# Performance work log

Hardware: AMD Instinct MI355X
Metric: run time of the kernel (lower is better)

## Reference

```python
import jax, jax.numpy as jnp
import numpy as np

N = 4096
HID = 512
NUM_HEADS = 8
HEAD_DIM = HID // NUM_HEADS
SCALING = HID ** (-0.5)


def setup_inputs() -> dict:
    key = jax.random.key(0)
    k0, k1, k2, k3, k4, k5 = jax.random.split(key, 6)
    h = jax.random.normal(k0, (N, HID), dtype=jnp.float32)
    A = (jax.random.uniform(k1, (N, N), dtype=jnp.float32) < 0.01).astype(jnp.float32)
    scale = 0.02
    Wq = jax.random.normal(k2, (HID, HID), dtype=jnp.float32) * scale
    Wk = jax.random.normal(k3, (HID, HID), dtype=jnp.float32) * scale
    Wv = jax.random.normal(k4, (HID, HID), dtype=jnp.float32) * scale
    Wo = jax.random.normal(k5, (HID, HID), dtype=jnp.float32) * scale
    return {"A": A, "h": h, "Wq": Wq, "Wk": Wk, "Wv": Wv, "Wo": Wo}


def reference(A, h, Wq, Wk, Wv, Wo):
    n = h.shape[0]
    # nn.Linear: y = x @ W.T ; reshape(N, head_dim, num_heads) puts heads LAST
    q = (h @ Wq.T).reshape(n, HEAD_DIM, NUM_HEADS) * SCALING  # [N, D, H]
    k = (h @ Wk.T).reshape(n, HEAD_DIM, NUM_HEADS)            # [N, D, H]
    v = (h @ Wv.T).reshape(n, HEAD_DIM, NUM_HEADS)            # [N, D, H]
    # scores = bmm(q^T[H,N,D], k^T[H,D,N]) -> [H, N, N]
    scores = jnp.einsum('ndh,mdh->hnm', q, k)
    # mask by dense multiply (zeros still contribute exp(0) to softmax, as in source)
    attn = jax.nn.softmax(A[None, :, :] * scores, axis=-1)    # [H, N, N]
    # out = bmm(attn, v^T[H,N,D]) -> [H, N, D] -> transpose to [N, D, H]
    out = jnp.einsum('hnm,mdh->ndh', attn, v)                 # [N, D, H]
    out = out.reshape(n, HEAD_DIM * NUM_HEADS) @ Wo.T         # [N, HID]
    return out
```

## Files before the change

### kernel.cpp

```cpp
#include <hip/hip_runtime.h>
#include <hip/hip_bf16.h>


#define N_TOK 4096
#define HID   512
#define NHEAD 8
#define HDIM  64
#define SCALING_F 0.044194173824159216f

#define QH_OFF    0u
#define KVB_OFF   2097152u
#define VSP_OFF   3145728u
#define VSUM_OFF  3162112u
#define CNT_OFF   3162624u
#define LIST_OFF  3166720u
#define HB_OFF    3691008u
#define WQKV_OFF  4739584u
#define WO_OFF    5132800u

typedef __attribute__((ext_vector_type(8))) short bf16x8;
typedef __attribute__((ext_vector_type(4))) float f32x4;
typedef __attribute__((ext_vector_type(2))) float f32x2;

__device__ __forceinline__ ushort f2bf(float f) {
    union { float f; unsigned u; } x; x.f = f;
    const unsigned r = x.u + 0x7fffu + ((x.u >> 16) & 1u);
    return (ushort)(r >> 16);
}

#define GLOAD_LDS16(g, l) \
    __builtin_amdgcn_global_load_lds((const __attribute__((address_space(1))) void*)(g), \
                                     (__attribute__((address_space(3))) void*)(l), 16, 0, 0)

__global__ __launch_bounds__(256) void prep(const float* __restrict__ A,
                                            const float* __restrict__ h,
                                            const float* __restrict__ wq,
                                            const float* __restrict__ wk,
                                            const float* __restrict__ wv,
                                            const float* __restrict__ wo,
                                            float* __restrict__ ws)
{
    const int bx = blockIdx.x;
    if (bx < 1024) {
        int* cnts  = (int*)(ws + CNT_OFF);
        int* lists = (int*)(ws + LIST_OFF);
        const int row  = bx * 4 + (threadIdx.x >> 6);
        const int lane = threadIdx.x & 63;
        const float4* Arow = (const float4*)(A + (size_t)row * N_TOK);
        int* out = lists + (size_t)row * 128;
        int cnt = 0;
#pragma unroll 4
        for (int it = 0; it < 16; ++it) {
            const float4 v = Arow[it * 64 + lane];
            const float vals[4] = {v.x, v.y, v.z, v.w};
#pragma unroll
            for (int j = 0; j < 4; ++j) {
                const bool nz = (vals[j] != 0.0f);
                const unsigned long long mask = __ballot(nz);
                if (nz) {
                    const int pos = cnt + __popcll(mask & ((1ull << lane) - 1ull));
                    if (pos < 128) out[pos] = it * 256 + lane * 4 + j;
                }
                cnt += __popcll(mask);
            }
        }
        if (lane == 0) cnts[row] = (cnt < 128) ? cnt : 128;
        return;
    }

    const int cb    = bx - 1024;
    const int chunk = cb >> 8;
    const int inner = (cb & 255) * 1024 + threadIdx.x * 4;
    ushort* hb    = (ushort*)(ws + HB_OFF);
    ushort* wqkvb = (ushort*)(ws + WQKV_OFF);
    ushort* wob   = (ushort*)(ws + WO_OFF);

    if (chunk < 11) {
        const float* src;
        ushort* dst;
        if (chunk < 8)       { src = h + (size_t)chunk * 262144; dst = hb + (size_t)chunk * 262144; }
        else if (chunk == 8) { src = wq; dst = wqkvb; }
        else if (chunk == 9) { src = wk; dst = wqkvb + 262144; }
        else                 { src = wv; dst = wqkvb + 524288; }
        const float4 v = *(const float4*)&src[inner];
        ushort4 o;
        o.x = f2bf(v.x); o.y = f2bf(v.y); o.z = f2bf(v.z); o.w = f2bf(v.w);
        *(ushort4*)&dst[inner] = o;
    } else {
        const float4 v = *(const float4*)&wo[inner];
        const int o = inner >> 9;
        const int j0 = inner & 511;
        const float vals[4] = {v.x, v.y, v.z, v.w};
#pragma unroll
        for (int jj = 0; jj < 4; ++jj) {
            const int j = j0 + jj;
            wob[o * 512 + (j & 7) * 64 + (j >> 3)] = f2bf(vals[jj]);
        }
    }
}

__global__ __launch_bounds__(256) void qkv_gemm_mfma(const float* __restrict__ ws_ro,
                                                     float* __restrict__ ws)
{
    const ushort* Xb = (const ushort*)(ws_ro + HB_OFF);
    const int z = blockIdx.z;
    const int hh = blockIdx.x;
    const ushort* W = (const ushort*)(ws_ro + WQKV_OFF) + (size_t)z * 262144;

    const int mb = blockIdx.y * 128;

    __shared__ ushort SM[12288];

    const int t    = threadIdx.x;
    const int w    = t >> 6;
    const int lane = t & 63;
    const int wr   = w >> 1, wc = w & 1;
    const int fr   = lane & 15;
    const int fq   = lane >> 4;
    const int fk   = fq * 8;

    const int srow = w * 16 + (lane >> 2);
    const int scol = (lane & 3) * 8;
    const ushort* gA = Xb + (size_t)(mb + srow) * HID + scol;
    const ushort* gB = W + (size_t)(hh + srow * 8) * HID + scol;

#define QKV_STAGE(p, kb) do { \
        ushort* base_ = &SM[(p) * 6144]; \
        GLOAD_LDS16(gA + (kb),            base_ + w * 512); \
        GLOAD_LDS16(gA + (kb) + 64 * HID, base_ + 2048 + w * 512); \
        GLOAD_LDS16(gB + (kb),            base_ + 4096 + w * 512); \
    } while (0)

    f32x4 acc[4][2] = {};

    QKV_STAGE(0, 0);
    __syncthreads();
    for (int ts = 0; ts < 16; ++ts) {
        const int p = ts & 1;
        if (ts < 15) QKV_STAGE(p ^ 1, (ts + 1) * 32);
        const ushort* base = &SM[p * 6144];
        bf16x8 a[4], b[2];
#pragma unroll
        for (int mi = 0; mi < 4; ++mi)
            a[mi] = *(const bf16x8*)&base[(wr * 64 + mi * 16 + fr) * 32 + fk];
#pragma unroll
        for (int ni = 0; ni < 2; ++ni)
            b[ni] = *(const bf16x8*)&base[4096 + (wc * 32 + ni * 16 + fr) * 32 + fk];
#pragma unroll
        for (int mi = 0; mi < 4; ++mi)
#pragma unroll
            for (int ni = 0; ni < 2; ++ni)
                acc[mi][ni] = __builtin_amdgcn_mfma_f32_16x16x32_bf16(a[mi], b[ni], acc[mi][ni], 0, 0, 0);
        __syncthreads();
    }
#undef QKV_STAGE

    if (z == 0) {
        float* Yh = ws + QH_OFF + (size_t)hh * (N_TOK * HDIM);
#pragma unroll
        for (int ni = 0; ni < 2; ++ni) {
            const int d = wc * 32 + ni * 16 + fr;
#pragma unroll
            for (int mi = 0; mi < 4; ++mi) {
                const int r0 = mb + wr * 64 + mi * 16 + fq * 4;
#pragma unroll
                for (int j = 0; j < 4; ++j)
                    Yh[(size_t)(r0 + j) * HDIM + d] = acc[mi][ni][j] * SCALING_F;
            }
        }
    } else {
        unsigned char* KVh = (unsigned char*)(ws + KVB_OFF)
                           + (size_t)hh * (N_TOK * 128) + ((z == 1) ? 0 : 8);
#pragma unroll
        for (int ni = 0; ni < 2; ++ni) {
            const int d = wc * 32 + ni * 16 + fr;
            const int doff = (d >> 3) * 16 + (d & 7);
#pragma unroll
            for (int mi = 0; mi < 4; ++mi) {
                const int r0 = mb + wr * 64 + mi * 16 + fq * 4;
#pragma unroll
                for (int j = 0; j < 4; ++j) {
                    const float v = acc[mi][ni][j];
                    const int p = __builtin_amdgcn_cvt_pk_fp8_f32(v, v, 0, false);
                    KVh[(size_t)(r0 + j) * 128 + doff] = (unsigned char)(p & 0xff);
                }
            }
        }
        if (z == 2) {
            float* red = (float*)SM;
#pragma unroll
            for (int ni = 0; ni < 2; ++ni) {
                float ps = 0.f;
#pragma unroll
                for (int mi = 0; mi < 4; ++mi)
#pragma unroll
                    for (int j = 0; j < 4; ++j) ps += acc[mi][ni][j];
                red[(wr * 4 + fq) * 64 + wc * 32 + ni * 16 + fr] = ps;
            }
            __syncthreads();
            if (t < 64) {
                float s = 0.f;
#pragma unroll
                for (int r = 0; r < 8; ++r) s += red[r * 64 + t];
                ws[VSP_OFF + blockIdx.y * 512 + hh * 64 + t] = s;
            }
        }
    }
}

__global__ __launch_bounds__(64) void vsum_collapse(float* __restrict__ ws)
{
    const float* VSP = ws + VSP_OFF;
    const int hh = blockIdx.x, d = threadIdx.x;
    float s = 0.f;
#pragma unroll
    for (int mb = 0; mb < 32; ++mb) s += VSP[mb * 512 + hh * 64 + d];
    ws[VSUM_OFF + hh * 64 + d] = s;
}

__global__ __launch_bounds__(256) void attn_sparse(float* __restrict__ ws)
{
    const int b    = blockIdx.x;
    const int n    = (b >> 3) * 4 + (b & 3);
    const int hg   = (b >> 2) & 1;
    const int t    = threadIdx.x;
    const int w    = t >> 6;
    const int lane = t & 63;
    const int g    = lane >> 3;
    const int dg   = lane & 7;
    const int h    = hg * 4 + w;

    const int* cnts  = (const int*)(ws + CNT_OFF);
    const int* lists = (const int*)(ws + LIST_OFF);

    __shared__ int s_idx[128];
    const int cnt = cnts[n];
    if (t < 128) s_idx[t] = (t < cnt) ? lists[(size_t)n * 128 + t] : 0;
    __syncthreads();

    const float* Qh = ws + QH_OFF;
    const unsigned char* kvh = (const unsigned char*)(ws + KVB_OFF)
                             + (size_t)h * (N_TOK * 128) + dg * 16;
    ushort* opb = (ushort*)(ws + HB_OFF);

    const float* qrow = Qh + ((size_t)h * N_TOK + n) * HDIM + dg * 8;
    const float4 qa = *(const float4*)qrow;
    const float4 qb = *(const float4*)(qrow + 4);

    float acc[8] = {0.f, 0.f, 0.f, 0.f, 0.f, 0.f, 0.f, 0.f};
    float den = 0.f;

    const int iters = (cnt + 7) >> 3;

#define ATTN_DOT(kw0, kw1, sval) do { \
        const f32x2 k0_ = __builtin_amdgcn_cvt_pk_f32_fp8((kw0), false); \
        const f32x2 k1_ = __builtin_amdgcn_cvt_pk_f32_fp8((kw0), true);  \
        const f32x2 k2_ = __builtin_amdgcn_cvt_pk_f32_fp8((kw1), false); \
        const f32x2 k3_ = __builtin_amdgcn_cvt_pk_f32_fp8((kw1), true);  \
        sval = qa.x * k0_[0] + qa.y * k0_[1] + qa.z * k1_[0] + qa.w * k1_[1] \
             + qb.x * k2_[0] + qb.y * k2_[1] + qb.z * k3_[0] + qb.w * k3_[1]; \
        sval += __shfl_xor(sval, 1); \
        sval += __shfl_xor(sval, 2); \
        sval += __shfl_xor(sval, 4); \
    } while (0)

#define ATTN_ACC(vw0, vw1, wgt) do { \
        const f32x2 v0_ = __builtin_amdgcn_cvt_pk_f32_fp8((vw0), false); \
        const f32x2 v1_ = __builtin_amdgcn_cvt_pk_f32_fp8((vw0), true);  \
        const f32x2 v2_ = __builtin_amdgcn_cvt_pk_f32_fp8((vw1), false); \
        const f32x2 v3_ = __builtin_amdgcn_cvt_pk_f32_fp8((vw1), true);  \
        acc[0] += (wgt) * v0_[0]; acc[1] += (wgt) * v0_[1]; \
        acc[2] += (wgt) * v1_[0]; acc[3] += (wgt) * v1_[1]; \
        acc[4] += (wgt) * v2_[0]; acc[5] += (wgt) * v2_[1]; \
        acc[6] += (wgt) * v3_[0]; acc[7] += (wgt) * v3_[1]; \
    } while (0)

    int i = 0;
    for (; i + 2 <= iters; i += 2) {
        const int j0 = i * 8 + g;
        const int j1 = j0 + 8;
        const int m0 = s_idx[j0];
        const int m1 = s_idx[j1];
        const uint4 kv0 = *(const uint4*)(kvh + (size_t)m0 * 128);
        const uint4 kv1 = *(const uint4*)(kvh + (size_t)m1 * 128);
        float s0, s1;
        ATTN_DOT(kv0.x, kv0.y, s0);
        ATTN_DOT(kv1.x, kv1.y, s1);
        const float w0 = (j0 < cnt) ? __expf(s0) - 1.0f : 0.0f;
        const float w1 = (j1 < cnt) ? __expf(s1) - 1.0f : 0.0f;
        ATTN_ACC(kv0.z, kv0.w, w0);
        ATTN_ACC(kv1.z, kv1.w, w1);
        den += w0;
        den += w1;
    }
    if (i < iters) {
        const int j0 = i * 8 + g;
        const int m0 = s_idx[j0 & 127];
        const uint4 kv0 = *(const uint4*)(kvh + (size_t)m0 * 128);
        float s0;
        ATTN_DOT(kv0.x, kv0.y, s0);
        const float w0 = (j0 < cnt) ? __expf(s0) - 1.0f : 0.0f;
        ATTN_ACC(kv0.z, kv0.w, w0);
        den += w0;
    }
#undef ATTN_DOT
#undef ATTN_ACC

#pragma unroll
    for (int off = 8; off <= 32; off <<= 1) {
#pragma unroll
        for (int e = 0; e < 8; ++e) acc[e] += __shfl_xor(acc[e], off);
        den += __shfl_xor(den, off);
    }

    if (g == 0) {
        const float* vsp = ws + VSUM_OFF + h * 64 + dg * 8;
        const float4 va = *(const float4*)vsp;
        const float4 vb = *(const float4*)(vsp + 4);
        const float vs[8] = {va.x, va.y, va.z, va.w, vb.x, vb.y, vb.z, vb.w};
        const float r = 1.0f / (4096.0f + den);
        bf16x8 o;
#pragma unroll
        for (int e = 0; e < 8; ++e) o[e] = (short)f2bf((vs[e] + acc[e]) * r);
        *(bf16x8*)(opb + (size_t)n * HID + h * 64 + dg * 8) = o;
    }
}

__global__ __launch_bounds__(256) void out_gemm_mfma(const float* __restrict__ ws_ro,
                                                     float* __restrict__ out)
{
    const ushort* Xb = (const ushort*)(ws_ro + HB_OFF);
    const ushort* W  = (const ushort*)(ws_ro + WO_OFF);

    const int nb = blockIdx.x * 64;
    const int mb = blockIdx.y * 128;

    __shared__ ushort SM[12288];

    const int t    = threadIdx.x;
    const int w    = t >> 6;
    const int lane = t & 63;
    const int wr   = w >> 1, wc = w & 1;
    const int fr   = lane & 15;
    const int fq   = lane >> 4;
    const int fk   = fq * 8;

    const int srow = w * 16 + (lane >> 2);
    const int scol = (lane & 3) * 8;
    const ushort* gA = Xb + (size_t)(mb + srow) * HID + scol;
    const ushort* gB = W  + (size_t)(nb + srow) * HID + scol;

#define OUT_STAGE(p, kb) do { \
        ushort* base_ = &SM[(p) * 6144]; \
        GLOAD_LDS16(gA + (kb),            base_ + w * 512); \
        GLOAD_LDS16(gA + (kb) + 64 * HID, base_ + 2048 + w * 512); \
        GLOAD_LDS16(gB + (kb),            base_ + 4096 + w * 512); \
    } while (0)

    f32x4 acc[4][2] = {};

    OUT_STAGE(0, 0);
    __syncthreads();
    for (int ts = 0; ts < 16; ++ts) {
        const int p = ts & 1;
        if (ts < 15) OUT_STAGE(p ^ 1, (ts + 1) * 32);
        const ushort* base = &SM[p * 6144];
        bf16x8 a[4], b[2];
#pragma unroll
        for (int mi = 0; mi < 4; ++mi)
            a[mi] = *(const bf16x8*)&base[(wr * 64 + mi * 16 + fr) * 32 + fk];
#pragma unroll
        for (int ni = 0; ni < 2; ++ni)
            b[ni] = *(const bf16x8*)&base[4096 + (wc * 32 + ni * 16 + fr) * 32 + fk];
#pragma unroll
        for (int mi = 0; mi < 4; ++mi)
#pragma unroll
            for (int ni = 0; ni < 2; ++ni)
                acc[mi][ni] = __builtin_amdgcn_mfma_f32_16x16x32_bf16(a[mi], b[ni], acc[mi][ni], 0, 0, 0);
        __syncthreads();
    }
#undef OUT_STAGE

#pragma unroll
    for (int ni = 0; ni < 2; ++ni) {
        const int col = nb + wc * 32 + ni * 16 + fr;
#pragma unroll
        for (int mi = 0; mi < 4; ++mi) {
            const int r0 = mb + wr * 64 + mi * 16 + fq * 4;
#pragma unroll
            for (int j = 0; j < 4; ++j)
                out[(size_t)(r0 + j) * HID + col] = acc[mi][ni][j];
        }
    }
}

extern "C" void kernel_launch(void* const* d_in, const int* in_sizes, int n_in,
                              void* d_out, int out_size, void* d_ws, size_t ws_size,
                              hipStream_t stream)
{
    const float* A  = (const float*)d_in[0];
    const float* h  = (const float*)d_in[1];
    const float* Wq = (const float*)d_in[2];
    const float* Wk = (const float*)d_in[3];
    const float* Wv = (const float*)d_in[4];
    const float* Wo = (const float*)d_in[5];
    float* out = (float*)d_out;
    float* ws  = (float*)d_ws;

    prep<<<dim3(4096), 256, 0, stream>>>(A, h, Wq, Wk, Wv, Wo, ws);
    qkv_gemm_mfma<<<dim3(8, 32, 3), 256, 0, stream>>>(ws, ws);
    vsum_collapse<<<dim3(8), 64, 0, stream>>>(ws);
    attn_sparse<<<dim3(8192), 256, 0, stream>>>(ws);
    out_gemm_mfma<<<dim3(8, 32), 256, 0, stream>>>(ws, out);
}
```

Before: 68.51 us.

## Fuse adjacency scan into QKV GEMM launch and fold V-sum via last-block reduction

Moves the 64 MB adjacency row scan out of the prep kernel and into extra blocks of the QKV GEMM launch, so the memory-bound scan overlaps with MFMA compute. The scan reads A with nontemporal loads. The separate vsum_collapse launch is removed: the last z==2 block, detected with an atomic counter and threadfences, reduces the partial sums. Q is prescaled by log2(e) so attention can use exp2f in place of __expf. This removes one launch and adds an atomic/fence path and a counter reset in prep.

Measured after the change: 129.4 us. 1.89x slower.

```diff
diff --git a/kernel.cpp b/kernel.cpp
--- a/kernel.cpp
+++ b/kernel.cpp
@@ -7,6 +7,7 @@
 #define NHEAD 8
 #define HDIM  64
 #define SCALING_F 0.044194173824159216f
+#define QSCALE_F  0.06376070971402051f
 
 #define QH_OFF    0u
 #define KVB_OFF   2097152u
@@ -17,6 +18,7 @@
 #define HB_OFF    3691008u
 #define WQKV_OFF  4739584u
 #define WO_OFF    5132800u
+#define CTR_OFF   5263872u
 
 typedef __attribute__((ext_vector_type(8))) short bf16x8;
 typedef __attribute__((ext_vector_type(4))) float f32x4;
@@ -32,8 +34,7 @@
     __builtin_amdgcn_global_load_lds((const __attribute__((address_space(1))) void*)(g), \
                                      (__attribute__((address_space(3))) void*)(l), 16, 0, 0)
 
-__global__ __launch_bounds__(256) void prep(const float* __restrict__ A,
-                                            const float* __restrict__ h,
+__global__ __launch_bounds__(256) void prep(const float* __restrict__ h,
                                             const float* __restrict__ wq,
                                             const float* __restrict__ wk,
                                             const float* __restrict__ wv,
@@ -41,36 +42,10 @@
                                             float* __restrict__ ws)
 {
     const int bx = blockIdx.x;
-    if (bx < 1024) {
-        int* cnts  = (int*)(ws + CNT_OFF);
-        int* lists = (int*)(ws + LIST_OFF);
-        const int row  = bx * 4 + (threadIdx.x >> 6);
-        const int lane = threadIdx.x & 63;
-        const float4* Arow = (const float4*)(A + (size_t)row * N_TOK);
-        int* out = lists + (size_t)row * 128;
-        int cnt = 0;
-#pragma unroll 4
-        for (int it = 0; it < 16; ++it) {
-            const float4 v = Arow[it * 64 + lane];
-            const float vals[4] = {v.x, v.y, v.z, v.w};
-#pragma unroll
-            for (int j = 0; j < 4; ++j) {
-                const bool nz = (vals[j] != 0.0f);
-                const unsigned long long mask = __ballot(nz);
-                if (nz) {
-                    const int pos = cnt + __popcll(mask & ((1ull << lane) - 1ull));
-                    if (pos < 128) out[pos] = it * 256 + lane * 4 + j;
-                }
-                cnt += __popcll(mask);
-            }
-        }
-        if (lane == 0) cnts[row] = (cnt < 128) ? cnt : 128;
-        return;
-    }
-
-    const int cb    = bx - 1024;
-    const int chunk = cb >> 8;
-    const int inner = (cb & 255) * 1024 + threadIdx.x * 4;
+    if (bx == 0 && threadIdx.x == 0) *(int*)(ws + CTR_OFF) = 0;
+
+    const int chunk = bx >> 8;
+    const int inner = (bx & 255) * 1024 + threadIdx.x * 4;
     ushort* hb    = (ushort*)(ws + HB_OFF);
     ushort* wqkvb = (ushort*)(ws + WQKV_OFF);
     ushort* wob   = (ushort*)(ws + WO_OFF);
@@ -99,19 +74,51 @@
     }
 }
 
-__global__ __launch_bounds__(256) void qkv_gemm_mfma(const float* __restrict__ ws_ro,
-                                                     float* __restrict__ ws)
+__global__ __launch_bounds__(256) void qkv_scan_fused(const float* __restrict__ A,
+                                                      const float* __restrict__ ws_ro,
+                                                      float* __restrict__ ws)
 {
+    const int bx = blockIdx.x;
+    const int t  = threadIdx.x;
+
+    if (bx >= 768) {
+        int* cnts  = (int*)(ws + CNT_OFF);
+        int* lists = (int*)(ws + LIST_OFF);
+        const int row  = (bx - 768) * 4 + (t >> 6);
+        const int lane = t & 63;
+        const f32x4* Arow = (const f32x4*)(A + (size_t)row * N_TOK);
+        int* out = lists + (size_t)row * 128;
+        int cnt = 0;
+#pragma unroll 4
+        for (int it = 0; it < 16; ++it) {
+            const f32x4 v = __builtin_nontemporal_load(&Arow[it * 64 + lane]);
+            const float vals[4] = {v.x, v.y, v.z, v.w};
+#pragma unroll
+            for (int j = 0; j < 4; ++j) {
+                const bool nz = (vals[j] != 0.0f);
+                const unsigned long long mask = __ballot(nz);
+                if (nz) {
+                    const int pos = cnt + __popcll(mask & ((1ull << lane) - 1ull));
+                    if (pos < 128) out[pos] = it * 256 + lane * 4 + j;
+                }
+                cnt += __popcll(mask);
+            }
+        }
+        if (lane == 0) cnts[row] = (cnt < 128) ? cnt : 128;
+        return;
+    }
+
     const ushort* Xb = (const ushort*)(ws_ro + HB_OFF);
-    const int z = blockIdx.z;
-    const int hh = blockIdx.x;
+    const int z   = bx >> 8;
+    const int rem = bx & 255;
+    const int hh  = rem & 7;
+    const int mbi = rem >> 3;
+    const int mb  = mbi * 128;
     const ushort* W = (const ushort*)(ws_ro + WQKV_OFF) + (size_t)z * 262144;
 
-    const int mb = blockIdx.y * 128;
-
     __shared__ ushort SM[12288];
-
-    const int t    = threadIdx.x;
+    __shared__ int s_last;
+
     const int w    = t >> 6;
     const int lane = t & 63;
     const int wr   = w >> 1, wc = w & 1;
@@ -165,7 +172,7 @@
                 const int r0 = mb + wr * 64 + mi * 16 + fq * 4;
 #pragma unroll
                 for (int j = 0; j < 4; ++j)
-                    Yh[(size_t)(r0 + j) * HDIM + d] = acc[mi][ni][j] * SCALING_F;
+                    Yh[(size_t)(r0 + j) * HDIM + d] = acc[mi][ni][j] * QSCALE_F;
             }
         }
     } else {
@@ -188,6 +195,7 @@
         }
         if (z == 2) {
             float* red = (float*)SM;
+            __syncthreads();
 #pragma unroll
             for (int ni = 0; ni < 2; ++ni) {
                 float ps = 0.f;
@@ -202,20 +210,27 @@
                 float s = 0.f;
 #pragma unroll
                 for (int r = 0; r < 8; ++r) s += red[r * 64 + t];
-                ws[VSP_OFF + blockIdx.y * 512 + hh * 64 + t] = s;
-            }
-        }
-    }
-}
-
-__global__ __launch_bounds__(64) void vsum_collapse(float* __restrict__ ws)
-{
-    const float* VSP = ws + VSP_OFF;
-    const int hh = blockIdx.x, d = threadIdx.x;
-    float s = 0.f;
-#pragma unroll
-    for (int mb = 0; mb < 32; ++mb) s += VSP[mb * 512 + hh * 64 + d];
-    ws[VSUM_OFF + hh * 64 + d] = s;
+                ws[VSP_OFF + mbi * 512 + hh * 64 + t] = s;
+            }
+            __syncthreads();
+            __threadfence();
+            if (t == 0) {
+                const int old = atomicAdd((int*)(ws + CTR_OFF), 1);
+                s_last = (old == 255) ? 1 : 0;
+            }
+            __syncthreads();
+            if (s_last) {
+                __threadfence();
+                for (int c = t; c < 512; c += 256) {
+                    float s = 0.f;
+#pragma unroll
+                    for (int mbp = 0; mbp < 32; ++mbp)
+                        s += ws[VSP_OFF + mbp * 512 + c];
+                    ws[VSUM_OFF + c] = s;
+                }
+            }
+        }
+    }
 }
 
 __global__ __launch_bounds__(256) void attn_sparse(float* __restrict__ ws)
@@ -286,8 +301,8 @@
         float s0, s1;
         ATTN_DOT(kv0.x, kv0.y, s0);
         ATTN_DOT(kv1.x, kv1.y, s1);
-        const float w0 = (j0 < cnt) ? __expf(s0) - 1.0f : 0.0f;
-        const float w1 = (j1 < cnt) ? __expf(s1) - 1.0f : 0.0f;
+        const float w0 = (j0 < cnt) ? exp2f(s0) - 1.0f : 0.0f;
+        const float w1 = (j1 < cnt) ? exp2f(s1) - 1.0f : 0.0f;
         ATTN_ACC(kv0.z, kv0.w, w0);
         ATTN_ACC(kv1.z, kv1.w, w1);
         den += w0;
@@ -299,7 +314,7 @@
         const uint4 kv0 = *(const uint4*)(kvh + (size_t)m0 * 128);
         float s0;
         ATTN_DOT(kv0.x, kv0.y, s0);
-        const float w0 = (j0 < cnt) ? __expf(s0) - 1.0f : 0.0f;
+        const float w0 = (j0 < cnt) ? exp2f(s0) - 1.0f : 0.0f;
         ATTN_ACC(kv0.z, kv0.w, w0);
         den += w0;
     }
@@ -407,9 +422,8 @@
     float* out = (float*)d_out;
     float* ws  = (float*)d_ws;
 
-    prep<<<dim3(4096), 256, 0, stream>>>(A, h, Wq, Wk, Wv, Wo, ws);
-    qkv_gemm_mfma<<<dim3(8, 32, 3), 256, 0, stream>>>(ws, ws);
-    vsum_collapse<<<dim3(8), 64, 0, stream>>>(ws);
+    prep<<<dim3(3072), 256, 0, stream>>>(h, Wq, Wk, Wv, Wo, ws);
+    qkv_scan_fused<<<dim3(1792), 256, 0, stream>>>(A, ws, ws);
     attn_sparse<<<dim3(8192), 256, 0, stream>>>(ws);
     out_gemm_mfma<<<dim3(8, 32), 256, 0, stream>>>(ws, out);
 }
```

## Drop LDS double buffering in GEMMs and fold log2e into Q scale for exp2

Applied to the files above, without the earlier changes.

Both MFMA GEMM kernels lose their double-buffered LDS staging and now use a single buffer with a sync before and after each load. LDS use per block drops, which could raise occupancy, but the next tile's global load no longer overlaps with compute. Separately, the Q scaling constant now includes log2(e), so the attention kernel can call exp2f instead of __expf.

Result: slower. 71.82 us (+4.8%).

```diff
diff --git a/kernel.cpp b/kernel.cpp
--- a/kernel.cpp
+++ b/kernel.cpp
@@ -6,7 +6,7 @@
 #define HID   512
 #define NHEAD 8
 #define HDIM  64
-#define SCALING_F 0.044194173824159216f
+#define QSCALE_F  0.06376070971402051f
 
 #define QH_OFF    0u
 #define KVB_OFF   2097152u
@@ -103,13 +103,14 @@
                                                      float* __restrict__ ws)
 {
     const ushort* Xb = (const ushort*)(ws_ro + HB_OFF);
-    const int z = blockIdx.z;
-    const int hh = blockIdx.x;
+    const int z   = blockIdx.z;
+    const int hh  = blockIdx.x;
+    const int mbi = blockIdx.y;
+    const int mb  = mbi * 128;
     const ushort* W = (const ushort*)(ws_ro + WQKV_OFF) + (size_t)z * 262144;
 
-    const int mb = blockIdx.y * 128;
-
-    __shared__ ushort SM[12288];
+    __shared__ ushort As[128 * 32];
+    __shared__ ushort Bs[64 * 32];
 
     const int t    = threadIdx.x;
     const int w    = t >> 6;
@@ -123,37 +124,31 @@
     const int scol = (lane & 3) * 8;
     const ushort* gA = Xb + (size_t)(mb + srow) * HID + scol;
     const ushort* gB = W + (size_t)(hh + srow * 8) * HID + scol;
-
-#define QKV_STAGE(p, kb) do { \
-        ushort* base_ = &SM[(p) * 6144]; \
-        GLOAD_LDS16(gA + (kb),            base_ + w * 512); \
-        GLOAD_LDS16(gA + (kb) + 64 * HID, base_ + 2048 + w * 512); \
-        GLOAD_LDS16(gB + (kb),            base_ + 4096 + w * 512); \
-    } while (0)
+    ushort* lAbase = &As[w * 512];
+    ushort* lBbase = &Bs[w * 512];
 
     f32x4 acc[4][2] = {};
 
-    QKV_STAGE(0, 0);
-    __syncthreads();
-    for (int ts = 0; ts < 16; ++ts) {
-        const int p = ts & 1;
-        if (ts < 15) QKV_STAGE(p ^ 1, (ts + 1) * 32);
-        const ushort* base = &SM[p * 6144];
+    for (int kb = 0; kb < HID; kb += 32) {
+        __syncthreads();
+        GLOAD_LDS16(gA + kb,            lAbase);
+        GLOAD_LDS16(gA + kb + 64 * HID, lAbase + 2048);
+        GLOAD_LDS16(gB + kb,            lBbase);
+        __syncthreads();
+
         bf16x8 a[4], b[2];
 #pragma unroll
         for (int mi = 0; mi < 4; ++mi)
-            a[mi] = *(const bf16x8*)&base[(wr * 64 + mi * 16 + fr) * 32 + fk];
+            a[mi] = *(const bf16x8*)&As[(wr * 64 + mi * 16 + fr) * 32 + fk];
 #pragma unroll
         for (int ni = 0; ni < 2; ++ni)
-            b[ni] = *(const bf16x8*)&base[4096 + (wc * 32 + ni * 16 + fr) * 32 + fk];
+            b[ni] = *(const bf16x8*)&Bs[(wc * 32 + ni * 16 + fr) * 32 + fk];
 #pragma unroll
         for (int mi = 0; mi < 4; ++mi)
 #pragma unroll
             for (int ni = 0; ni < 2; ++ni)
                 acc[mi][ni] = __builtin_amdgcn_mfma_f32_16x16x32_bf16(a[mi], b[ni], acc[mi][ni], 0, 0, 0);
-        __syncthreads();
-    }
-#undef QKV_STAGE
+    }
 
     if (z == 0) {
         float* Yh = ws + QH_OFF + (size_t)hh * (N_TOK * HDIM);
@@ -165,7 +160,7 @@
                 const int r0 = mb + wr * 64 + mi * 16 + fq * 4;
 #pragma unroll
                 for (int j = 0; j < 4; ++j)
-                    Yh[(size_t)(r0 + j) * HDIM + d] = acc[mi][ni][j] * SCALING_F;
+                    Yh[(size_t)(r0 + j) * HDIM + d] = acc[mi][ni][j] * QSCALE_F;
             }
         }
     } else {
@@ -187,7 +182,8 @@
             }
         }
         if (z == 2) {
-            float* red = (float*)SM;
+            __syncthreads();
+            float* red = (float*)As;
 #pragma unroll
             for (int ni = 0; ni < 2; ++ni) {
                 float ps = 0.f;
@@ -202,7 +198,7 @@
                 float s = 0.f;
 #pragma unroll
                 for (int r = 0; r < 8; ++r) s += red[r * 64 + t];
-                ws[VSP_OFF + blockIdx.y * 512 + hh * 64 + t] = s;
+                ws[VSP_OFF + mbi * 512 + hh * 64 + t] = s;
             }
         }
     }
@@ -286,8 +282,8 @@
         float s0, s1;
         ATTN_DOT(kv0.x, kv0.y, s0);
         ATTN_DOT(kv1.x, kv1.y, s1);
-        const float w0 = (j0 < cnt) ? __expf(s0) - 1.0f : 0.0f;
-        const float w1 = (j1 < cnt) ? __expf(s1) - 1.0f : 0.0f;
+        const float w0 = (j0 < cnt) ? exp2f(s0) - 1.0f : 0.0f;
+        const float w1 = (j1 < cnt) ? exp2f(s1) - 1.0f : 0.0f;
         ATTN_ACC(kv0.z, kv0.w, w0);
         ATTN_ACC(kv1.z, kv1.w, w1);
         den += w0;
@@ -299,7 +295,7 @@
         const uint4 kv0 = *(const uint4*)(kvh + (size_t)m0 * 128);
         float s0;
         ATTN_DOT(kv0.x, kv0.y, s0);
-        const float w0 = (j0 < cnt) ? __expf(s0) - 1.0f : 0.0f;
+        const float w0 = (j0 < cnt) ? exp2f(s0) - 1.0f : 0.0f;
         ATTN_ACC(kv0.z, kv0.w, w0);
         den += w0;
     }
@@ -335,7 +331,8 @@
     const int nb = blockIdx.x * 64;
     const int mb = blockIdx.y * 128;
 
-    __shared__ ushort SM[12288];
+    __shared__ ushort As[128 * 32];
+    __shared__ ushort Bs[64 * 32];
 
     const int t    = threadIdx.x;
     const int w    = t >> 6;
@@ -349,37 +346,31 @@
     const int scol = (lane & 3) * 8;
     const ushort* gA = Xb + (size_t)(mb + srow) * HID + scol;
     const ushort* gB = W  + (size_t)(nb + srow) * HID + scol;
-
-#define OUT_STAGE(p, kb) do { \
-        ushort* base_ = &SM[(p) * 6144]; \
-        GLOAD_LDS16(gA + (kb),            base_ + w * 512); \
-        GLOAD_LDS16(gA + (kb) + 64 * HID, base_ + 2048 + w * 512); \
-        GLOAD_LDS16(gB + (kb),            base_ + 4096 + w * 512); \
-    } while (0)
+    ushort* lAbase = &As[w * 512];
+    ushort* lBbase = &Bs[w * 512];
 
     f32x4 acc[4][2] = {};
 
-    OUT_STAGE(0, 0);
-    __syncthreads();
-    for (int ts = 0; ts < 16; ++ts) {
-        const int p = ts & 1;
-        if (ts < 15) OUT_STAGE(p ^ 1, (ts + 1) * 32);
-        const ushort* base = &SM[p * 6144];
+    for (int kb = 0; kb < HID; kb += 32) {
+        __syncthreads();
+        GLOAD_LDS16(gA + kb,            lAbase);
+        GLOAD_LDS16(gA + kb + 64 * HID, lAbase + 2048);
+        GLOAD_LDS16(gB + kb,            lBbase);
+        __syncthreads();
+
         bf16x8 a[4], b[2];
 #pragma unroll
         for (int mi = 0; mi < 4; ++mi)
-            a[mi] = *(const bf16x8*)&base[(wr * 64 + mi * 16 + fr) * 32 + fk];
+            a[mi] = *(const bf16x8*)&As[(wr * 64 + mi * 16 + fr) * 32 + fk];
 #pragma unroll
         for (int ni = 0; ni < 2; ++ni)
-            b[ni] = *(const bf16x8*)&base[4096 + (wc * 32 + ni * 16 + fr) * 32 + fk];
+            b[ni] = *(const bf16x8*)&Bs[(wc * 32 + ni * 16 + fr) * 32 + fk];
 #pragma unroll
         for (int mi = 0; mi < 4; ++mi)
 #pragma unroll
             for (int ni = 0; ni < 2; ++ni)
                 acc[mi][ni] = __builtin_amdgcn_mfma_f32_16x16x32_bf16(a[mi], b[ni], acc[mi][ni], 0, 0, 0);
-        __syncthreads();
-    }
-#undef OUT_STAGE
+    }
 
 #pragma unroll
     for (int ni = 0; ni < 2; ++ni) {
```

## Fuse Q/K/V projections into one GEMM block sharing the activation tile

Applied to the files above, without the earlier changes.

The QKV GEMM no longer launches a separate z-slice per projection. Each block now loads the activation tile once and computes Q, K and V against three weight tiles, which triples the accumulators and grows shared memory to 40KB. This cuts redundant activation loads and shrinks the grid from 768 to 256 blocks, which risks lower occupancy and parallelism. Separately, Q is pre-scaled by log2(e) so the attention kernel can use exp2f in place of __expf.

Measured after the change: 73.37 us. +7.1%, slower.

```diff
diff --git a/kernel.cpp b/kernel.cpp
--- a/kernel.cpp
+++ b/kernel.cpp
@@ -6,7 +6,7 @@
 #define HID   512
 #define NHEAD 8
 #define HDIM  64
-#define SCALING_F 0.044194173824159216f
+#define QSCALE_F  0.06376070971402051f
 
 #define QH_OFF    0u
 #define KVB_OFF   2097152u
@@ -103,13 +103,12 @@
                                                      float* __restrict__ ws)
 {
     const ushort* Xb = (const ushort*)(ws_ro + HB_OFF);
-    const int z = blockIdx.z;
-    const int hh = blockIdx.x;
-    const ushort* W = (const ushort*)(ws_ro + WQKV_OFF) + (size_t)z * 262144;
-
-    const int mb = blockIdx.y * 128;
-
-    __shared__ ushort SM[12288];
+    const int hh  = blockIdx.x;
+    const int mbi = blockIdx.y;
+    const int mb  = mbi * 128;
+    const ushort* Wb = (const ushort*)(ws_ro + WQKV_OFF);
+
+    __shared__ ushort SM[2 * 10240];
 
     const int t    = threadIdx.x;
     const int w    = t >> 6;
@@ -121,41 +120,49 @@
 
     const int srow = w * 16 + (lane >> 2);
     const int scol = (lane & 3) * 8;
-    const ushort* gA = Xb + (size_t)(mb + srow) * HID + scol;
-    const ushort* gB = W + (size_t)(hh + srow * 8) * HID + scol;
+    const ushort* gA  = Xb + (size_t)(mb + srow) * HID + scol;
+    const ushort* gB0 = Wb + (size_t)(hh + srow * 8) * HID + scol;
+    const ushort* gB1 = gB0 + 262144;
+    const ushort* gB2 = gB0 + 524288;
 
 #define QKV_STAGE(p, kb) do { \
-        ushort* base_ = &SM[(p) * 6144]; \
-        GLOAD_LDS16(gA + (kb),            base_ + w * 512); \
-        GLOAD_LDS16(gA + (kb) + 64 * HID, base_ + 2048 + w * 512); \
-        GLOAD_LDS16(gB + (kb),            base_ + 4096 + w * 512); \
+        ushort* base_ = &SM[(p) * 10240]; \
+        GLOAD_LDS16(gA  + (kb),            base_ + w * 512); \
+        GLOAD_LDS16(gA  + (kb) + 64 * HID, base_ + 2048 + w * 512); \
+        GLOAD_LDS16(gB0 + (kb),            base_ + 4096 + w * 512); \
+        GLOAD_LDS16(gB1 + (kb),            base_ + 6144 + w * 512); \
+        GLOAD_LDS16(gB2 + (kb),            base_ + 8192 + w * 512); \
     } while (0)
 
-    f32x4 acc[4][2] = {};
+    f32x4 acc[3][4][2] = {};
 
     QKV_STAGE(0, 0);
     __syncthreads();
     for (int ts = 0; ts < 16; ++ts) {
         const int p = ts & 1;
         if (ts < 15) QKV_STAGE(p ^ 1, (ts + 1) * 32);
-        const ushort* base = &SM[p * 6144];
-        bf16x8 a[4], b[2];
+        const ushort* base = &SM[p * 10240];
+        bf16x8 a[4], b[3][2];
 #pragma unroll
         for (int mi = 0; mi < 4; ++mi)
             a[mi] = *(const bf16x8*)&base[(wr * 64 + mi * 16 + fr) * 32 + fk];
 #pragma unroll
-        for (int ni = 0; ni < 2; ++ni)
-            b[ni] = *(const bf16x8*)&base[4096 + (wc * 32 + ni * 16 + fr) * 32 + fk];
-#pragma unroll
-        for (int mi = 0; mi < 4; ++mi)
+        for (int z = 0; z < 3; ++z)
 #pragma unroll
             for (int ni = 0; ni < 2; ++ni)
-                acc[mi][ni] = __builtin_amdgcn_mfma_f32_16x16x32_bf16(a[mi], b[ni], acc[mi][ni], 0, 0, 0);
+                b[z][ni] = *(const bf16x8*)&base[4096 + z * 2048 + (wc * 32 + ni * 16 + fr) * 32 + fk];
+#pragma unroll
+        for (int z = 0; z < 3; ++z)
+#pragma unroll
+            for (int mi = 0; mi < 4; ++mi)
+#pragma unroll
+                for (int ni = 0; ni < 2; ++ni)
+                    acc[z][mi][ni] = __builtin_amdgcn_mfma_f32_16x16x32_bf16(a[mi], b[z][ni], acc[z][mi][ni], 0, 0, 0);
         __syncthreads();
     }
 #undef QKV_STAGE
 
-    if (z == 0) {
+    {
         float* Yh = ws + QH_OFF + (size_t)hh * (N_TOK * HDIM);
 #pragma unroll
         for (int ni = 0; ni < 2; ++ni) {
@@ -165,45 +172,50 @@
                 const int r0 = mb + wr * 64 + mi * 16 + fq * 4;
 #pragma unroll
                 for (int j = 0; j < 4; ++j)
-                    Yh[(size_t)(r0 + j) * HDIM + d] = acc[mi][ni][j] * SCALING_F;
+                    Yh[(size_t)(r0 + j) * HDIM + d] = acc[0][mi][ni][j] * QSCALE_F;
             }
         }
-    } else {
-        unsigned char* KVh = (unsigned char*)(ws + KVB_OFF)
-                           + (size_t)hh * (N_TOK * 128) + ((z == 1) ? 0 : 8);
-#pragma unroll
-        for (int ni = 0; ni < 2; ++ni) {
-            const int d = wc * 32 + ni * 16 + fr;
-            const int doff = (d >> 3) * 16 + (d & 7);
-#pragma unroll
-            for (int mi = 0; mi < 4; ++mi) {
-                const int r0 = mb + wr * 64 + mi * 16 + fq * 4;
-#pragma unroll
-                for (int j = 0; j < 4; ++j) {
-                    const float v = acc[mi][ni][j];
-                    const int p = __builtin_amdgcn_cvt_pk_fp8_f32(v, v, 0, false);
-                    KVh[(size_t)(r0 + j) * 128 + doff] = (unsigned char)(p & 0xff);
+    }
+    {
+        unsigned char* KVh = (unsigned char*)(ws + KVB_OFF) + (size_t)hh * (N_TOK * 128);
+#pragma unroll
+        for (int z = 1; z < 3; ++z) {
+            const int off = (z == 1) ? 0 : 8;
+#pragma unroll
+            for (int ni = 0; ni < 2; ++ni) {
+                const int d = wc * 32 + ni * 16 + fr;
+                const int doff = (d >> 3) * 16 + (d & 7) + off;
+#pragma unroll
+                for (int mi = 0; mi < 4; ++mi) {
+                    const int r0 = mb + wr * 64 + mi * 16 + fq * 4;
+#pragma unroll
+                    for (int j = 0; j < 4; ++j) {
+                        const float v = acc[z][mi][ni][j];
+                        const int pk = __builtin_amdgcn_cvt_pk_fp8_f32(v, v, 0, false);
+                        KVh[(size_t)(r0 + j) * 128 + doff] = (unsigned char)(pk & 0xff);
+                    }
                 }
             }
         }
-        if (z == 2) {
-            float* red = (float*)SM;
-#pragma unroll
-            for (int ni = 0; ni < 2; ++ni) {
-                float ps = 0.f;
-#pragma unroll
-                for (int mi = 0; mi < 4; ++mi)
-#pragma unroll
-                    for (int j = 0; j < 4; ++j) ps += acc[mi][ni][j];
-                red[(wr * 4 + fq) * 64 + wc * 32 + ni * 16 + fr] = ps;
-            }
-            __syncthreads();
-            if (t < 64) {
-                float s = 0.f;
-#pragma unroll
-                for (int r = 0; r < 8; ++r) s += red[r * 64 + t];
-                ws[VSP_OFF + blockIdx.y * 512 + hh * 64 + t] = s;
-            }
+    }
+    {
+        __syncthreads();
+        float* red = (float*)SM;
+#pragma unroll
+        for (int ni = 0; ni < 2; ++ni) {
+            float ps = 0.f;
+#pragma unroll
+            for (int mi = 0; mi < 4; ++mi)
+#pragma unroll
+                for (int j = 0; j < 4; ++j) ps += acc[2][mi][ni][j];
+            red[(wr * 4 + fq) * 64 + wc * 32 + ni * 16 + fr] = ps;
+        }
+        __syncthreads();
+        if (t < 64) {
+            float s = 0.f;
+#pragma unroll
+            for (int r = 0; r < 8; ++r) s += red[r * 64 + t];
+            ws[VSP_OFF + mbi * 512 + hh * 64 + t] = s;
         }
     }
 }
@@ -286,8 +298,8 @@
         float s0, s1;
         ATTN_DOT(kv0.x, kv0.y, s0);
         ATTN_DOT(kv1.x, kv1.y, s1);
-        const float w0 = (j0 < cnt) ? __expf(s0) - 1.0f : 0.0f;
-        const float w1 = (j1 < cnt) ? __expf(s1) - 1.0f : 0.0f;
+        const float w0 = (j0 < cnt) ? exp2f(s0) - 1.0f : 0.0f;
+        const float w1 = (j1 < cnt) ? exp2f(s1) - 1.0f : 0.0f;
         ATTN_ACC(kv0.z, kv0.w, w0);
         ATTN_ACC(kv1.z, kv1.w, w1);
         den += w0;
@@ -299,7 +311,7 @@
         const uint4 kv0 = *(const uint4*)(kvh + (size_t)m0 * 128);
         float s0;
         ATTN_DOT(kv0.x, kv0.y, s0);
-        const float w0 = (j0 < cnt) ? __expf(s0) - 1.0f : 0.0f;
+        const float w0 = (j0 < cnt) ? exp2f(s0) - 1.0f : 0.0f;
         ATTN_ACC(kv0.z, kv0.w, w0);
         den += w0;
     }
@@ -408,7 +420,7 @@
     float* ws  = (float*)d_ws;
 
     prep<<<dim3(4096), 256, 0, stream>>>(A, h, Wq, Wk, Wv, Wo, ws);
-    qkv_gemm_mfma<<<dim3(8, 32, 3), 256, 0, stream>>>(ws, ws);
+    qkv_gemm_mfma<<<dim3(8, 32), 256, 0, stream>>>(ws, ws);
     vsum_collapse<<<dim3(8), 64, 0, stream>>>(ws);
     attn_sparse<<<dim3(8192), 256, 0, stream>>>(ws);
     out_gemm_mfma<<<dim3(8, 32), 256, 0, stream>>>(ws, out);
```
